# Optimization experiments

Hardware: AMD Instinct MI355X
Metric: run time of the kernel (lower is better)

The kernel has to match this reference:

```python
import jax, jax.numpy as jnp
import numpy as np

B, T, H, NH, K = 8, 1024, 1024, 16, 3
HD = H // NH
EPS = 1e-5


def _ln(x, g, b):
    m = jnp.mean(x, axis=-1, keepdims=True)
    v = jnp.mean((x - m) ** 2, axis=-1, keepdims=True)
    return (x - m) * jax.lax.rsqrt(v + EPS) * g + b


def _ffn(x, g, b, w1, b1, w2, b2):
    h = jax.nn.gelu(_ln(x, g, b) @ w1 + b1, approximate=False)
    return h @ w2 + b2


def setup_inputs() -> dict:
    key = jax.random.key(0)
    ks = jax.random.split(key, 10)
    s = 0.02
    d = {}
    d['x'] = jax.random.normal(ks[0], (B, T, H), jnp.float32)
    d['ln1_g'] = jnp.ones((H,), jnp.float32); d['ln1_b'] = jnp.zeros((H,), jnp.float32)
    d['ffn1_w1'] = jax.random.normal(ks[1], (H, 2 * H), jnp.float32) * s
    d['ffn1_b1'] = jnp.zeros((2 * H,), jnp.float32)
    d['ffn1_w2'] = jax.random.normal(ks[2], (2 * H, H), jnp.float32) * s
    d['ffn1_b2'] = jnp.zeros((H,), jnp.float32)
    d['an_g'] = jnp.ones((H,), jnp.float32); d['an_b'] = jnp.zeros((H,), jnp.float32)
    d['qkv_w'] = jax.random.normal(ks[3], (H, 3 * H), jnp.float32) * s
    d['qkv_b'] = jnp.zeros((3 * H,), jnp.float32)
    d['out_w'] = jax.random.normal(ks[4], (H, H), jnp.float32) * s
    d['out_b'] = jnp.zeros((H,), jnp.float32)
    d['cn_g'] = jnp.ones((H,), jnp.float32); d['cn_b'] = jnp.zeros((H,), jnp.float32)
    d['dw_k'] = jax.random.normal(ks[5], (H, 1, K), jnp.float32) * s  # depthwise [O,I/g,K]
    d['dw_b'] = jnp.zeros((H,), jnp.float32)
    d['pw_w'] = jax.random.normal(ks[6], (H, H), jnp.float32) * s  # pointwise [out,in]
    d['pw_b'] = jnp.zeros((H,), jnp.float32)
    d['ln2_g'] = jnp.ones((H,), jnp.float32); d['ln2_b'] = jnp.zeros((H,), jnp.float32)
    d['ffn2_w1'] = jax.random.normal(ks[7], (H, 2 * H), jnp.float32) * s
    d['ffn2_b1'] = jnp.zeros((2 * H,), jnp.float32)
    d['ffn2_w2'] = jax.random.normal(ks[8], (2 * H, H), jnp.float32) * s
    d['ffn2_b2'] = jnp.zeros((H,), jnp.float32)
    return d


def reference(x, ln1_g, ln1_b, ffn1_w1, ffn1_b1, ffn1_w2, ffn1_b2,
              an_g, an_b, qkv_w, qkv_b, out_w, out_b,
              cn_g, cn_b, dw_k, dw_b, pw_w, pw_b,
              ln2_g, ln2_b, ffn2_w1, ffn2_b1, ffn2_w2, ffn2_b2):
    # macaron FFN 1
    x = x + 0.5 * _ffn(x, ln1_g, ln1_b, ffn1_w1, ffn1_b1, ffn1_w2, ffn1_b2)

    # causal self-attention (pre-norm)
    h = _ln(x, an_g, an_b)
    qkv = (h @ qkv_w + qkv_b).reshape(B, T, 3, NH, HD)
    q, k, v = qkv[:, :, 0], qkv[:, :, 1], qkv[:, :, 2]  # [B,T,NH,HD]
    scale = 1.0 / np.sqrt(HD).astype(np.float32)
    scores = jnp.einsum('bqhd,bkhd->bhqk', q, k) * scale  # [B,NH,T,T]
    causal = jnp.tril(jnp.ones((T, T), dtype=bool))
    scores = jnp.where(causal[None, None], scores, -jnp.inf)
    attn = jax.nn.softmax(scores, axis=-1)
    o = jnp.einsum('bhqk,bkhd->bqhd', attn, v).reshape(B, T, H)
    x = x + (o @ out_w + out_b)

    # conv module: LN -> causal depthwise conv(k=3) -> GELU -> pointwise conv
    c = _ln(x, cn_g, cn_b).transpose(0, 2, 1)  # [B,H,T]
    c = jnp.pad(c, ((0, 0), (0, 0), (K - 1, 0)))  # causal left pad
    c = jax.lax.conv_general_dilated(
        c, dw_k, window_strides=(1,), padding='VALID',
        dimension_numbers=('NCH', 'OIH', 'NCH'), feature_group_count=H)
    c = c + dw_b[None, :, None]
    c = jax.nn.gelu(c, approximate=False)
    c = jnp.einsum('oc,bct->bot', pw_w, c) + pw_b[None, :, None]  # 1x1 conv
    x = x + c.transpose(0, 2, 1)

    # macaron FFN 2
    x = x + 0.5 * _ffn(x, ln2_g, ln2_b, ffn2_w1, ffn2_b1, ffn2_w2, ffn2_b2)
    return x
```

## Files before the change

### kernel.cpp

```cpp
#include <hip/hip_runtime.h>
#include <hip/hip_bf16.h>
#include <math.h>

typedef __bf16 bf16;
typedef __bf16 bf16x8 __attribute__((ext_vector_type(8)));
typedef float  f32x4  __attribute__((ext_vector_type(4)));

#define B_   8
#define T_   1024
#define H_   1024
#define MTOK (B_ * T_)

static __device__ __forceinline__ float gelu_f(float x) {
    return 0.5f * x * (1.0f + erff(x * 0.70710678118654752f));
}

static __device__ __forceinline__ void async16(const bf16* g, bf16* l) {
    __builtin_amdgcn_global_load_lds(
        (const __attribute__((address_space(1))) void*)g,
        (__attribute__((address_space(3))) void*)l, 16, 0, 0);
}

__global__ __launch_bounds__(256)
void transpose_cast_k(const float* __restrict__ in, bf16* __restrict__ out,
                      int Kd, int Nd)
{
    __shared__ float tile[32][33];
    int n0 = blockIdx.x * 32;
    int k0 = blockIdx.y * 32;
    int tx = threadIdx.x & 31, ty = threadIdx.x >> 5;
#pragma unroll
    for (int i = 0; i < 32; i += 8)
        tile[ty + i][tx] = in[(size_t)(k0 + ty + i) * Nd + n0 + tx];
    __syncthreads();
#pragma unroll
    for (int i = 0; i < 32; i += 8)
        out[(size_t)(n0 + ty + i) * Kd + k0 + tx] = (bf16)tile[tx][ty + i];
}

__global__ __launch_bounds__(256)
void cast_k(const float* __restrict__ in, bf16* __restrict__ out)
{
    int i = blockIdx.x * 256 + threadIdx.x;
    float4 v = ((const float4*)in)[i];
    bf16* o = out + (size_t)i * 4;
    o[0] = (bf16)v.x; o[1] = (bf16)v.y; o[2] = (bf16)v.z; o[3] = (bf16)v.w;
}

__global__ __launch_bounds__(256)
void transpose_v_k(const bf16* __restrict__ qkv, bf16* __restrict__ vt)
{
    __shared__ bf16 tile[64][72];
    const int t0 = blockIdx.x * 64;
    const int bh = blockIdx.y;
    const int b = bh >> 4, h = bh & 15;
    const int tid = threadIdx.x;
#pragma unroll
    for (int i = 0; i < 2; i++) {
        int c = tid + i * 256;
        int row = c >> 3, ch = (c & 7) << 3;
        *(bf16x8*)(&tile[row][ch]) =
            *(const bf16x8*)(&qkv[(size_t)(b * T_ + t0 + row) * 3072 + 2048 + h * 64 + ch]);
    }
    __syncthreads();
#pragma unroll
    for (int i = 0; i < 2; i++) {
        int c = tid + i * 256;
        int hd = c >> 3, tc = (c & 7) << 3;
        bf16x8 v;
#pragma unroll
        for (int j = 0; j < 8; j++) v[j] = tile[tc + j][hd];
        *(bf16x8*)(&vt[((size_t)bh * 64 + hd) * T_ + t0 + tc]) = v;
    }
}

__global__ __launch_bounds__(256)
void ln_k(const float* __restrict__ x, const float* __restrict__ g,
          const float* __restrict__ b, bf16* __restrict__ out)
{
    int row = blockIdx.x;
    float4 v = ((const float4*)(x + (size_t)row * H_))[threadIdx.x];
    float s  = v.x + v.y + v.z + v.w;
    float s2 = v.x * v.x + v.y * v.y + v.z * v.z + v.w * v.w;
#pragma unroll
    for (int off = 32; off > 0; off >>= 1) {
        s  += __shfl_down(s, off);
        s2 += __shfl_down(s2, off);
    }
    __shared__ float red[8];
    int wave = threadIdx.x >> 6, lane = threadIdx.x & 63;
    if (lane == 0) { red[wave] = s; red[wave + 4] = s2; }
    __syncthreads();
    s  = red[0] + red[1] + red[2] + red[3];
    s2 = red[4] + red[5] + red[6] + red[7];
    float mean = s * (1.0f / H_);
    float var  = s2 * (1.0f / H_) - mean * mean;
    float rstd = rsqrtf(var + 1e-5f);
    int c = threadIdx.x * 4;
    float4 gv = *(const float4*)(g + c);
    float4 bv = *(const float4*)(b + c);
    bf16* o = out + (size_t)row * H_ + c;
    o[0] = (bf16)((v.x - mean) * rstd * gv.x + bv.x);
    o[1] = (bf16)((v.y - mean) * rstd * gv.y + bv.y);
    o[2] = (bf16)((v.z - mean) * rstd * gv.z + bv.z);
    o[3] = (bf16)((v.w - mean) * rstd * gv.w + bv.w);
}

__global__ __launch_bounds__(256)
void dwconv_k(const bf16* __restrict__ cl, const float* __restrict__ kw,
              const float* __restrict__ kb, bf16* __restrict__ out)
{
    size_t idx = (size_t)blockIdx.x * 256 + threadIdx.x;
    int ch = (int)(idx & (H_ - 1));
    int t  = (int)((idx >> 10) & (T_ - 1));
    float acc = kb[ch];
    float w0 = kw[ch * 3 + 0], w1 = kw[ch * 3 + 1], w2 = kw[ch * 3 + 2];
    acc += (float)cl[idx] * w2;
    if (t >= 1) acc += (float)cl[idx - H_] * w1;
    if (t >= 2) acc += (float)cl[idx - 2 * H_] * w0;
    out[idx] = (bf16)gelu_f(acc);
}

template<int EPI>
__global__ __launch_bounds__(256)
void gemm_k(const bf16* __restrict__ A, const bf16* __restrict__ WT,
            const float* __restrict__ bias, const float* __restrict__ res,
            float* __restrict__ outF, bf16* __restrict__ outB,
            int N, int K)
{
    __shared__ __align__(16) bf16 As[2][128 * 32];
    __shared__ __align__(16) bf16 Bs[2][128 * 32];
    const int tid  = threadIdx.x;
    const int wave = tid >> 6;
    const int lane = tid & 63;
    const int quad = lane >> 4;
    const int lr   = lane & 15;
    const int bm = blockIdx.x * 128;
    const int bn = blockIdx.y * 128;
    const int wm = (wave & 1) * 64;
    const int wn = (wave >> 1) * 64;

    const int crow = lane >> 2;
    const int ccol = (lane & 3) << 3;

    auto stage = [&](int k0, int buf) {
#pragma unroll
        for (int t = 0; t < 2; t++) {
            const int c = wave * 2 + t;
            async16(&A[(size_t)(bm + c * 16 + crow) * K + k0 + ccol], &As[buf][c * 512]);
            async16(&WT[(size_t)(bn + c * 16 + crow) * K + k0 + ccol], &Bs[buf][c * 512]);
        }
    };

    f32x4 acc[4][4];
#pragma unroll
    for (int mi = 0; mi < 4; mi++)
#pragma unroll
        for (int ni = 0; ni < 4; ni++)
#pragma unroll
            for (int r = 0; r < 4; r++) acc[mi][ni][r] = 0.f;

    stage(0, 0);
    __syncthreads();
    const int nk = K >> 5;
    for (int ki = 0; ki < nk; ki++) {
        const int cur = ki & 1;
        if (ki + 1 < nk) stage((ki + 1) << 5, cur ^ 1);

        bf16x8 af[4], bfr[4];
#pragma unroll
        for (int mi = 0; mi < 4; mi++)
            af[mi] = *(const bf16x8*)(&As[cur][(wm + mi * 16 + lr) * 32 + quad * 8]);
#pragma unroll
        for (int ni = 0; ni < 4; ni++)
            bfr[ni] = *(const bf16x8*)(&Bs[cur][(wn + ni * 16 + lr) * 32 + quad * 8]);
#pragma unroll
        for (int mi = 0; mi < 4; mi++)
#pragma unroll
            for (int ni = 0; ni < 4; ni++)
                acc[mi][ni] = __builtin_amdgcn_mfma_f32_16x16x32_bf16(
                    af[mi], bfr[ni], acc[mi][ni], 0, 0, 0);
        __syncthreads();
    }

#pragma unroll
    for (int mi = 0; mi < 4; mi++) {
#pragma unroll
        for (int ni = 0; ni < 4; ni++) {
            int col = bn + wn + ni * 16 + lr;
            float bv = bias[col];
#pragma unroll
            for (int r = 0; r < 4; r++) {
                int row = bm + wm + mi * 16 + quad * 4 + r;
                size_t idx = (size_t)row * N + col;
                float v = acc[mi][ni][r] + bv;
                if (EPI == 0)      outB[idx] = (bf16)gelu_f(v);
                else if (EPI == 1) outB[idx] = (bf16)v;
                else if (EPI == 2) outF[idx] = v + res[idx];
                else               outF[idx] = res[idx] + 0.5f * v;
            }
        }
    }
}

template<int EPI>
__global__ __launch_bounds__(256)
void gemm64_k(const bf16* __restrict__ A, const bf16* __restrict__ WT,
              const float* __restrict__ bias, const float* __restrict__ res,
              float* __restrict__ outF, bf16* __restrict__ outB,
              int N, int K)
{
    __shared__ __align__(16) bf16 As[2][64 * 32];
    __shared__ __align__(16) bf16 Bs[2][128 * 32];
    const int tid  = threadIdx.x;
    const int wave = tid >> 6;
    const int lane = tid & 63;
    const int quad = lane >> 4;
    const int lr   = lane & 15;
    const int bm = blockIdx.x * 64;
    const int bn = blockIdx.y * 128;
    const int wm = (wave & 1) * 32;
    const int wn = (wave >> 1) * 64;

    const int crow = lane >> 2;
    const int ccol = (lane & 3) << 3;

    auto stage = [&](int k0, int buf) {
        async16(&A[(size_t)(bm + wave * 16 + crow) * K + k0 + ccol], &As[buf][wave * 512]);
#pragma unroll
        for (int t = 0; t < 2; t++) {
            const int c = wave * 2 + t;
            async16(&WT[(size_t)(bn + c * 16 + crow) * K + k0 + ccol], &Bs[buf][c * 512]);
        }
    };

    f32x4 acc[2][4];
#pragma unroll
    for (int mi = 0; mi < 2; mi++)
#pragma unroll
        for (int ni = 0; ni < 4; ni++)
#pragma unroll
            for (int r = 0; r < 4; r++) acc[mi][ni][r] = 0.f;

    stage(0, 0);
    __syncthreads();
    const int nk = K >> 5;
    for (int ki = 0; ki < nk; ki++) {
        const int cur = ki & 1;
        if (ki + 1 < nk) stage((ki + 1) << 5, cur ^ 1);

        bf16x8 af[2], bfr[4];
#pragma unroll
        for (int mi = 0; mi < 2; mi++)
            af[mi] = *(const bf16x8*)(&As[cur][(wm + mi * 16 + lr) * 32 + quad * 8]);
#pragma unroll
        for (int ni = 0; ni < 4; ni++)
            bfr[ni] = *(const bf16x8*)(&Bs[cur][(wn + ni * 16 + lr) * 32 + quad * 8]);
#pragma unroll
        for (int mi = 0; mi < 2; mi++)
#pragma unroll
            for (int ni = 0; ni < 4; ni++)
                acc[mi][ni] = __builtin_amdgcn_mfma_f32_16x16x32_bf16(
                    af[mi], bfr[ni], acc[mi][ni], 0, 0, 0);
        __syncthreads();
    }

#pragma unroll
    for (int mi = 0; mi < 2; mi++) {
#pragma unroll
        for (int ni = 0; ni < 4; ni++) {
            int col = bn + wn + ni * 16 + lr;
            float bv = bias[col];
#pragma unroll
            for (int r = 0; r < 4; r++) {
                int row = bm + wm + mi * 16 + quad * 4 + r;
                size_t idx = (size_t)row * N + col;
                float v = acc[mi][ni][r] + bv;
                if (EPI == 0)      outB[idx] = (bf16)gelu_f(v);
                else if (EPI == 1) outB[idx] = (bf16)v;
                else if (EPI == 2) outF[idx] = v + res[idx];
                else               outF[idx] = res[idx] + 0.5f * v;
            }
        }
    }
}

__global__ __launch_bounds__(256)
void attn_k(const bf16* __restrict__ qkv, const bf16* __restrict__ vt,
            bf16* __restrict__ o)
{
    const int B0 = blockIdx.x;
    const int bh = blockIdx.y;
    const int b = bh >> 4, h = bh & 15;
    const int tid  = threadIdx.x;
    const int wave = tid >> 6, lane = tid & 63;
    const int quad = lane >> 4, lr = lane & 15;

    __shared__ __align__(16) bf16 Ks[2][2][64 * 32];
    __shared__ __align__(16) bf16 Vs[2][2][64 * 32];
    __shared__ __align__(16) bf16 Ps[4][16 * 72];

    const int crow = lane >> 2;
    const int ccol = (lane & 3) << 3;

    const int qa = B0 * 128 + wave * 16;
    const int qb = qa + 64;

    bf16x8 qfa[2], qfb[2];
    {
        const size_t ra = ((size_t)(b * T_ + qa + lr)) * 3072 + h * 64;
        const size_t rb = ((size_t)(b * T_ + qb + lr)) * 3072 + h * 64;
        qfa[0] = *(const bf16x8*)(&qkv[ra + quad * 8]);
        qfa[1] = *(const bf16x8*)(&qkv[ra + 32 + quad * 8]);
        qfb[0] = *(const bf16x8*)(&qkv[rb + quad * 8]);
        qfb[1] = *(const bf16x8*)(&qkv[rb + 32 + quad * 8]);
#pragma unroll
        for (int j = 0; j < 8; j++) {
            qfa[0][j] = (bf16)((float)qfa[0][j] * 0.125f);
            qfa[1][j] = (bf16)((float)qfa[1][j] * 0.125f);
            qfb[0][j] = (bf16)((float)qfb[0][j] * 0.125f);
            qfb[1][j] = (bf16)((float)qfb[1][j] * 0.125f);
        }
    }

    f32x4 oa[4], ob[4];
    float la[4], lb[4];
#pragma unroll
    for (int ni = 0; ni < 4; ni++)
#pragma unroll
        for (int r = 0; r < 4; r++) { oa[ni][r] = 0.f; ob[ni][r] = 0.f; }
#pragma unroll
    for (int r = 0; r < 4; r++) { la[r] = 0.f; lb[r] = 0.f; }

    const size_t kbase = (size_t)b * T_ * 3072 + 1024 + h * 64;
    const size_t vbase = (size_t)bh * 64 * T_;

    auto stage = [&](int kt, int buf) {
#pragma unroll
        for (int half = 0; half < 2; half++) {
            async16(&qkv[kbase + (size_t)(kt * 64 + wave * 16 + crow) * 3072 + half * 32 + ccol],
                    &Ks[buf][half][wave * 512]);
            async16(&vt[vbase + (size_t)(wave * 16 + crow) * T_ + kt * 64 + half * 32 + ccol],
                    &Vs[buf][half][wave * 512]);
        }
    };

    const int ktmax = 2 * B0 + 1;
    stage(0, 0);
    __syncthreads();

    for (int kt = 0; kt <= ktmax; kt++) {
        const int cur = kt & 1;
        if (kt < ktmax) stage(kt + 1, cur ^ 1);

        bf16x8 kf[4][2], vf[4][2];
#pragma unroll
        for (int ni = 0; ni < 4; ni++) {
            kf[ni][0] = *(const bf16x8*)(&Ks[cur][0][(ni * 16 + lr) * 32 + quad * 8]);
            kf[ni][1] = *(const bf16x8*)(&Ks[cur][1][(ni * 16 + lr) * 32 + quad * 8]);
            vf[ni][0] = *(const bf16x8*)(&Vs[cur][0][(ni * 16 + lr) * 32 + quad * 8]);
            vf[ni][1] = *(const bf16x8*)(&Vs[cur][1][(ni * 16 + lr) * 32 + quad * 8]);
        }

        auto stripe = [&](const bf16x8 (&qf)[2], f32x4 (&oacc)[4], float (&lsum)[4],
                          int q0, bool diag) {
            f32x4 sv[4];
#pragma unroll
            for (int ni = 0; ni < 4; ni++) {
                f32x4 t;
#pragma unroll
                for (int r = 0; r < 4; r++) t[r] = 0.f;
                t = __builtin_amdgcn_mfma_f32_16x16x32_bf16(qf[0], kf[ni][0], t, 0, 0, 0);
                t = __builtin_amdgcn_mfma_f32_16x16x32_bf16(qf[1], kf[ni][1], t, 0, 0, 0);
                sv[ni] = t;
            }
            if (diag) {
#pragma unroll
                for (int ni = 0; ni < 4; ni++)
#pragma unroll
                    for (int r = 0; r < 4; r++)
                        if (kt * 64 + ni * 16 + lr > q0 + quad * 4 + r)
                            sv[ni][r] = -INFINITY;
            }
#pragma unroll
            for (int ni = 0; ni < 4; ni++)
#pragma unroll
                for (int r = 0; r < 4; r++) {
                    float p = __expf(sv[ni][r]);
                    lsum[r] += p;
                    Ps[wave][(quad * 4 + r) * 72 + ni * 16 + lr] = (bf16)p;
                }
            bf16x8 pf0 = *(const bf16x8*)(&Ps[wave][lr * 72 + quad * 8]);
            bf16x8 pf1 = *(const bf16x8*)(&Ps[wave][lr * 72 + 32 + quad * 8]);
#pragma unroll
            for (int ni = 0; ni < 4; ni++) {
                oacc[ni] = __builtin_amdgcn_mfma_f32_16x16x32_bf16(pf0, vf[ni][0], oacc[ni], 0, 0, 0);
                oacc[ni] = __builtin_amdgcn_mfma_f32_16x16x32_bf16(pf1, vf[ni][1], oacc[ni], 0, 0, 0);
            }
        };

        if (kt <= 2 * B0)
            stripe(qfa, oa, la, qa, kt == 2 * B0);
        stripe(qfb, ob, lb, qb, kt == ktmax);
        __syncthreads();
    }

#pragma unroll
    for (int off = 1; off < 16; off <<= 1)
#pragma unroll
        for (int r = 0; r < 4; r++) {
            la[r] += __shfl_xor(la[r], off);
            lb[r] += __shfl_xor(lb[r], off);
        }

#pragma unroll
    for (int r = 0; r < 4; r++) {
        float inva = 1.0f / la[r], invb = 1.0f / lb[r];
        int ga = qa + quad * 4 + r, gb = qb + quad * 4 + r;
#pragma unroll
        for (int ni = 0; ni < 4; ni++) {
            o[((size_t)(b * T_ + ga)) * H_ + h * 64 + ni * 16 + lr] = (bf16)(oa[ni][r] * inva);
            o[((size_t)(b * T_ + gb)) * H_ + h * 64 + ni * 16 + lr] = (bf16)(ob[ni][r] * invb);
        }
    }
}

extern "C" void kernel_launch(void* const* d_in, const int* in_sizes, int n_in,
                              void* d_out, int out_size, void* d_ws, size_t ws_size,
                              hipStream_t stream)
{
    const float* x_in  = (const float*)d_in[0];
    const float* ln1_g = (const float*)d_in[1];
    const float* ln1_b = (const float*)d_in[2];
    const float* f1w1  = (const float*)d_in[3];
    const float* f1b1  = (const float*)d_in[4];
    const float* f1w2  = (const float*)d_in[5];
    const float* f1b2  = (const float*)d_in[6];
    const float* an_g  = (const float*)d_in[7];
    const float* an_b  = (const float*)d_in[8];
    const float* qkv_w = (const float*)d_in[9];
    const float* qkv_b = (const float*)d_in[10];
    const float* out_w = (const float*)d_in[11];
    const float* out_b = (const float*)d_in[12];
    const float* cn_g  = (const float*)d_in[13];
    const float* cn_b  = (const float*)d_in[14];
    const float* dw_k  = (const float*)d_in[15];
    const float* dw_b  = (const float*)d_in[16];
    const float* pw_w  = (const float*)d_in[17];
    const float* pw_b  = (const float*)d_in[18];
    const float* ln2_g = (const float*)d_in[19];
    const float* ln2_b = (const float*)d_in[20];
    const float* f2w1  = (const float*)d_in[21];
    const float* f2b1  = (const float*)d_in[22];
    const float* f2w2  = (const float*)d_in[23];
    const float* f2b2  = (const float*)d_in[24];
    float* outp = (float*)d_out;

    char* ws = (char*)d_ws;
    size_t off = 0;
    auto alloc = [&](size_t bytes) {
        char* p = ws + off;
        off += (bytes + 255) & ~(size_t)255;
        return p;
    };
    bf16* w1T_1 = (bf16*)alloc(2048ULL * 1024 * 2);
    bf16* w2T_1 = (bf16*)alloc(1024ULL * 2048 * 2);
    bf16* qkvT  = (bf16*)alloc(3072ULL * 1024 * 2);
    bf16* outT  = (bf16*)alloc(1024ULL * 1024 * 2);
    bf16* pwB   = (bf16*)alloc(1024ULL * 1024 * 2);
    bf16* w1T_2 = (bf16*)alloc(2048ULL * 1024 * 2);
    bf16* w2T_2 = (bf16*)alloc(1024ULL * 2048 * 2);
    bf16* bufa  = (bf16*)alloc((size_t)MTOK * 1024 * 2);
    bf16* gbuf  = (bf16*)alloc((size_t)MTOK * 1024 * 2);
    bf16* hid   = (bf16*)alloc((size_t)MTOK * 3072 * 2);
    float* xw   = (float*)alloc((size_t)MTOK * 1024 * 4);
    bf16* vt    = gbuf;

    transpose_cast_k<<<dim3(64, 32), 256, 0, stream>>>(f1w1, w1T_1, 1024, 2048);
    transpose_cast_k<<<dim3(32, 64), 256, 0, stream>>>(f1w2, w2T_1, 2048, 1024);
    transpose_cast_k<<<dim3(96, 32), 256, 0, stream>>>(qkv_w, qkvT, 1024, 3072);
    transpose_cast_k<<<dim3(32, 32), 256, 0, stream>>>(out_w, outT, 1024, 1024);
    transpose_cast_k<<<dim3(64, 32), 256, 0, stream>>>(f2w1, w1T_2, 1024, 2048);
    transpose_cast_k<<<dim3(32, 64), 256, 0, stream>>>(f2w2, w2T_2, 2048, 1024);
    cast_k<<<1024, 256, 0, stream>>>(pw_w, pwB);

    ln_k<<<MTOK, 256, 0, stream>>>(x_in, ln1_g, ln1_b, bufa);
    gemm_k<0><<<dim3(64, 16), 256, 0, stream>>>(bufa, w1T_1, f1b1, nullptr, nullptr, hid, 2048, 1024);
    gemm64_k<3><<<dim3(128, 8), 256, 0, stream>>>(hid, w2T_1, f1b2, x_in, xw, nullptr, 1024, 2048);

    ln_k<<<MTOK, 256, 0, stream>>>(xw, an_g, an_b, bufa);
    gemm_k<1><<<dim3(64, 24), 256, 0, stream>>>(bufa, qkvT, qkv_b, nullptr, nullptr, hid, 3072, 1024);
    transpose_v_k<<<dim3(16, 128), 256, 0, stream>>>(hid, vt);
    attn_k<<<dim3(8, 128), 256, 0, stream>>>(hid, vt, bufa);
    gemm64_k<2><<<dim3(128, 8), 256, 0, stream>>>(bufa, outT, out_b, xw, xw, nullptr, 1024, 1024);

    ln_k<<<MTOK, 256, 0, stream>>>(xw, cn_g, cn_b, bufa);
    dwconv_k<<<MTOK * 1024 / 256, 256, 0, stream>>>(bufa, dw_k, dw_b, gbuf);
    gemm64_k<2><<<dim3(128, 8), 256, 0, stream>>>(gbuf, pwB, pw_b, xw, xw, nullptr, 1024, 1024);

    ln_k<<<MTOK, 256, 0, stream>>>(xw, ln2_g, ln2_b, bufa);
    gemm_k<0><<<dim3(64, 16), 256, 0, stream>>>(bufa, w1T_2, f2b1, nullptr, nullptr, hid, 2048, 1024);
    gemm64_k<3><<<dim3(128, 8), 256, 0, stream>>>(hid, w2T_2, f2b2, xw, outp, nullptr, 1024, 2048);
}
```

Baseline: 683.0 us.

## Fuse weight prep, write V transposed from QKV GEMM, restructure attention loop

Merges the seven weight transpose/cast launches into a single table-driven prep kernel. The QKV GEMM epilogue now writes V directly in transposed layout and pre-scales Q by 1/8, which removes the separate V-transpose kernel and the in-attention Q scaling. The attention kernel launches its heaviest causal blocks first. It also drops double-buffered K/V staging in favour of a single buffer with barriers around each load, which halves shared memory but exposes load latency.

```diff
diff --git a/kernel.cpp b/kernel.cpp
--- a/kernel.cpp
+++ b/kernel.cpp
@@ -3,6 +3,7 @@
 #include <math.h>
 
 typedef __bf16 bf16;
+typedef __bf16 bf16x4 __attribute__((ext_vector_type(4)));
 typedef __bf16 bf16x8 __attribute__((ext_vector_type(8)));
 typedef float  f32x4  __attribute__((ext_vector_type(4)));
 
@@ -21,56 +22,41 @@
         (__attribute__((address_space(3))) void*)l, 16, 0, 0);
 }
 
-__global__ __launch_bounds__(256)
-void transpose_cast_k(const float* __restrict__ in, bf16* __restrict__ out,
-                      int Kd, int Nd)
+struct PrepTab {
+    const float* in[7];
+    bf16*        out[7];
+    int kd[7], nd[7], mode[7];
+    int bx0[8];
+};
+
+__global__ __launch_bounds__(256)
+void prep_k(PrepTab tab)
 {
     __shared__ float tile[32][33];
-    int n0 = blockIdx.x * 32;
-    int k0 = blockIdx.y * 32;
-    int tx = threadIdx.x & 31, ty = threadIdx.x >> 5;
-#pragma unroll
-    for (int i = 0; i < 32; i += 8)
-        tile[ty + i][tx] = in[(size_t)(k0 + ty + i) * Nd + n0 + tx];
-    __syncthreads();
-#pragma unroll
-    for (int i = 0; i < 32; i += 8)
-        out[(size_t)(n0 + ty + i) * Kd + k0 + tx] = (bf16)tile[tx][ty + i];
-}
-
-__global__ __launch_bounds__(256)
-void cast_k(const float* __restrict__ in, bf16* __restrict__ out)
-{
-    int i = blockIdx.x * 256 + threadIdx.x;
-    float4 v = ((const float4*)in)[i];
-    bf16* o = out + (size_t)i * 4;
-    o[0] = (bf16)v.x; o[1] = (bf16)v.y; o[2] = (bf16)v.z; o[3] = (bf16)v.w;
-}
-
-__global__ __launch_bounds__(256)
-void transpose_v_k(const bf16* __restrict__ qkv, bf16* __restrict__ vt)
-{
-    __shared__ bf16 tile[64][72];
-    const int t0 = blockIdx.x * 64;
-    const int bh = blockIdx.y;
-    const int b = bh >> 4, h = bh & 15;
-    const int tid = threadIdx.x;
-#pragma unroll
-    for (int i = 0; i < 2; i++) {
-        int c = tid + i * 256;
-        int row = c >> 3, ch = (c & 7) << 3;
-        *(bf16x8*)(&tile[row][ch]) =
-            *(const bf16x8*)(&qkv[(size_t)(b * T_ + t0 + row) * 3072 + 2048 + h * 64 + ch]);
-    }
-    __syncthreads();
-#pragma unroll
-    for (int i = 0; i < 2; i++) {
-        int c = tid + i * 256;
-        int hd = c >> 3, tc = (c & 7) << 3;
-        bf16x8 v;
-#pragma unroll
-        for (int j = 0; j < 8; j++) v[j] = tile[tc + j][hd];
-        *(bf16x8*)(&vt[((size_t)bh * 64 + hd) * T_ + t0 + tc]) = v;
+    int bx = blockIdx.x;
+    int j = 0;
+    while (bx >= tab.bx0[j + 1]) j++;
+    int local = bx - tab.bx0[j];
+    const float* in = tab.in[j];
+    bf16* out = tab.out[j];
+    if (tab.mode[j] == 0) {
+        int Kd = tab.kd[j], Nd = tab.nd[j];
+        int nbn = Nd >> 5;
+        int n0 = (local % nbn) * 32;
+        int k0 = (local / nbn) * 32;
+        int tx = threadIdx.x & 31, ty = threadIdx.x >> 5;
+#pragma unroll
+        for (int i = 0; i < 32; i += 8)
+            tile[ty + i][tx] = in[(size_t)(k0 + ty + i) * Nd + n0 + tx];
+        __syncthreads();
+#pragma unroll
+        for (int i = 0; i < 32; i += 8)
+            out[(size_t)(n0 + ty + i) * Kd + k0 + tx] = (bf16)tile[tx][ty + i];
+    } else {
+        size_t i = (size_t)local * 1024 + threadIdx.x * 4;
+        float4 v = *(const float4*)(in + i);
+        bf16* o = out + i;
+        o[0] = (bf16)v.x; o[1] = (bf16)v.y; o[2] = (bf16)v.z; o[3] = (bf16)v.w;
     }
 }
 
@@ -126,7 +112,7 @@
 void gemm_k(const bf16* __restrict__ A, const bf16* __restrict__ WT,
             const float* __restrict__ bias, const float* __restrict__ res,
             float* __restrict__ outF, bf16* __restrict__ outB,
-            int N, int K)
+            bf16* __restrict__ vtp, int N, int K)
 {
     __shared__ __align__(16) bf16 As[2][128 * 32];
     __shared__ __align__(16) bf16 Bs[2][128 * 32];
@@ -189,15 +175,27 @@
         for (int ni = 0; ni < 4; ni++) {
             int col = bn + wn + ni * 16 + lr;
             float bv = bias[col];
-#pragma unroll
-            for (int r = 0; r < 4; r++) {
-                int row = bm + wm + mi * 16 + quad * 4 + r;
-                size_t idx = (size_t)row * N + col;
-                float v = acc[mi][ni][r] + bv;
-                if (EPI == 0)      outB[idx] = (bf16)gelu_f(v);
-                else if (EPI == 1) outB[idx] = (bf16)v;
-                else if (EPI == 2) outF[idx] = v + res[idx];
-                else               outF[idx] = res[idx] + 0.5f * v;
+            if (EPI == 4 && col >= 2048) {
+                int vcol = col - 2048;
+                int hh = vcol >> 6, hd = vcol & 63;
+                int rowbase = bm + wm + mi * 16 + quad * 4;
+                int bq = rowbase >> 10, t0 = rowbase & 1023;
+                bf16x4 tmp;
+#pragma unroll
+                for (int r = 0; r < 4; r++) tmp[r] = (bf16)(acc[mi][ni][r] + bv);
+                *(bf16x4*)(&vtp[((size_t)((bq * 16 + hh) * 64 + hd)) * T_ + t0]) = tmp;
+            } else {
+#pragma unroll
+                for (int r = 0; r < 4; r++) {
+                    int row = bm + wm + mi * 16 + quad * 4 + r;
+                    size_t idx = (size_t)row * N + col;
+                    float v = acc[mi][ni][r] + bv;
+                    if (EPI == 0)      outB[idx] = (bf16)gelu_f(v);
+                    else if (EPI == 1) outB[idx] = (bf16)v;
+                    else if (EPI == 2) outF[idx] = v + res[idx];
+                    else if (EPI == 3) outF[idx] = res[idx] + 0.5f * v;
+                    else               outB[idx] = (bf16)(col < 1024 ? v * 0.125f : v);
+                }
             }
         }
     }
@@ -289,15 +287,15 @@
 void attn_k(const bf16* __restrict__ qkv, const bf16* __restrict__ vt,
             bf16* __restrict__ o)
 {
-    const int B0 = blockIdx.x;
+    const int B0 = 7 - blockIdx.x;
     const int bh = blockIdx.y;
     const int b = bh >> 4, h = bh & 15;
     const int tid  = threadIdx.x;
     const int wave = tid >> 6, lane = tid & 63;
     const int quad = lane >> 4, lr = lane & 15;
 
-    __shared__ __align__(16) bf16 Ks[2][2][64 * 32];
-    __shared__ __align__(16) bf16 Vs[2][2][64 * 32];
+    __shared__ __align__(16) bf16 Ks[2][64 * 32];
+    __shared__ __align__(16) bf16 Vs[2][64 * 32];
     __shared__ __align__(16) bf16 Ps[4][16 * 72];
 
     const int crow = lane >> 2;
@@ -314,13 +312,6 @@
         qfa[1] = *(const bf16x8*)(&qkv[ra + 32 + quad * 8]);
         qfb[0] = *(const bf16x8*)(&qkv[rb + quad * 8]);
         qfb[1] = *(const bf16x8*)(&qkv[rb + 32 + quad * 8]);
-#pragma unroll
-        for (int j = 0; j < 8; j++) {
-            qfa[0][j] = (bf16)((float)qfa[0][j] * 0.125f);
-            qfa[1][j] = (bf16)((float)qfa[1][j] * 0.125f);
-            qfb[0][j] = (bf16)((float)qfb[0][j] * 0.125f);
-            qfb[1][j] = (bf16)((float)qfb[1][j] * 0.125f);
-        }
     }
 
     f32x4 oa[4], ob[4];
@@ -335,74 +326,65 @@
     const size_t kbase = (size_t)b * T_ * 3072 + 1024 + h * 64;
     const size_t vbase = (size_t)bh * 64 * T_;
 
-    auto stage = [&](int kt, int buf) {
+    auto stripe = [&](const bf16x8 (&qf)[2], f32x4 (&oacc)[4], float (&lsum)[4],
+                      int q0, int kcol0, bool diag) {
+        bf16x8 kf0[4], kf1[4];
+#pragma unroll
+        for (int ni = 0; ni < 4; ni++) {
+            kf0[ni] = *(const bf16x8*)(&Ks[0][(ni * 16 + lr) * 32 + quad * 8]);
+            kf1[ni] = *(const bf16x8*)(&Ks[1][(ni * 16 + lr) * 32 + quad * 8]);
+        }
+        f32x4 sv[4];
+#pragma unroll
+        for (int ni = 0; ni < 4; ni++) {
+            f32x4 t;
+#pragma unroll
+            for (int r = 0; r < 4; r++) t[r] = 0.f;
+            t = __builtin_amdgcn_mfma_f32_16x16x32_bf16(qf[0], kf0[ni], t, 0, 0, 0);
+            t = __builtin_amdgcn_mfma_f32_16x16x32_bf16(qf[1], kf1[ni], t, 0, 0, 0);
+            sv[ni] = t;
+        }
+        if (diag) {
+#pragma unroll
+            for (int ni = 0; ni < 4; ni++)
+#pragma unroll
+                for (int r = 0; r < 4; r++)
+                    if (kcol0 + ni * 16 + lr > q0 + quad * 4 + r)
+                        sv[ni][r] = -INFINITY;
+        }
+#pragma unroll
+        for (int ni = 0; ni < 4; ni++)
+#pragma unroll
+            for (int r = 0; r < 4; r++) {
+                float p = __expf(sv[ni][r]);
+                lsum[r] += p;
+                Ps[wave][(quad * 4 + r) * 72 + ni * 16 + lr] = (bf16)p;
+            }
+        bf16x8 pf0 = *(const bf16x8*)(&Ps[wave][lr * 72 + quad * 8]);
+        bf16x8 pf1 = *(const bf16x8*)(&Ps[wave][lr * 72 + 32 + quad * 8]);
+#pragma unroll
+        for (int ni = 0; ni < 4; ni++) {
+            bf16x8 vf0 = *(const bf16x8*)(&Vs[0][(ni * 16 + lr) * 32 + quad * 8]);
+            bf16x8 vf1 = *(const bf16x8*)(&Vs[1][(ni * 16 + lr) * 32 + quad * 8]);
+            oacc[ni] = __builtin_amdgcn_mfma_f32_16x16x32_bf16(pf0, vf0, oacc[ni], 0, 0, 0);
+            oacc[ni] = __builtin_amdgcn_mfma_f32_16x16x32_bf16(pf1, vf1, oacc[ni], 0, 0, 0);
+        }
+    };
+
+    const int ktmax = 2 * B0 + 1;
+    for (int kt = 0; kt <= ktmax; kt++) {
+        __syncthreads();
 #pragma unroll
         for (int half = 0; half < 2; half++) {
             async16(&qkv[kbase + (size_t)(kt * 64 + wave * 16 + crow) * 3072 + half * 32 + ccol],
-                    &Ks[buf][half][wave * 512]);
+                    &Ks[half][wave * 512]);
             async16(&vt[vbase + (size_t)(wave * 16 + crow) * T_ + kt * 64 + half * 32 + ccol],
-                    &Vs[buf][half][wave * 512]);
-        }
-    };
-
-    const int ktmax = 2 * B0 + 1;
-    stage(0, 0);
-    __syncthreads();
-
-    for (int kt = 0; kt <= ktmax; kt++) {
-        const int cur = kt & 1;
-        if (kt < ktmax) stage(kt + 1, cur ^ 1);
-
-        bf16x8 kf[4][2], vf[4][2];
-#pragma unroll
-        for (int ni = 0; ni < 4; ni++) {
-            kf[ni][0] = *(const bf16x8*)(&Ks[cur][0][(ni * 16 + lr) * 32 + quad * 8]);
-            kf[ni][1] = *(const bf16x8*)(&Ks[cur][1][(ni * 16 + lr) * 32 + quad * 8]);
-            vf[ni][0] = *(const bf16x8*)(&Vs[cur][0][(ni * 16 + lr) * 32 + quad * 8]);
-            vf[ni][1] = *(const bf16x8*)(&Vs[cur][1][(ni * 16 + lr) * 32 + quad * 8]);
-        }
-
-        auto stripe = [&](const bf16x8 (&qf)[2], f32x4 (&oacc)[4], float (&lsum)[4],
-                          int q0, bool diag) {
-            f32x4 sv[4];
-#pragma unroll
-            for (int ni = 0; ni < 4; ni++) {
-                f32x4 t;
-#pragma unroll
-                for (int r = 0; r < 4; r++) t[r] = 0.f;
-                t = __builtin_amdgcn_mfma_f32_16x16x32_bf16(qf[0], kf[ni][0], t, 0, 0, 0);
-                t = __builtin_amdgcn_mfma_f32_16x16x32_bf16(qf[1], kf[ni][1], t, 0, 0, 0);
-                sv[ni] = t;
-            }
-            if (diag) {
-#pragma unroll
-                for (int ni = 0; ni < 4; ni++)
-#pragma unroll
-                    for (int r = 0; r < 4; r++)
-                        if (kt * 64 + ni * 16 + lr > q0 + quad * 4 + r)
-                            sv[ni][r] = -INFINITY;
-            }
-#pragma unroll
-            for (int ni = 0; ni < 4; ni++)
-#pragma unroll
-                for (int r = 0; r < 4; r++) {
-                    float p = __expf(sv[ni][r]);
-                    lsum[r] += p;
-                    Ps[wave][(quad * 4 + r) * 72 + ni * 16 + lr] = (bf16)p;
-                }
-            bf16x8 pf0 = *(const bf16x8*)(&Ps[wave][lr * 72 + quad * 8]);
-            bf16x8 pf1 = *(const bf16x8*)(&Ps[wave][lr * 72 + 32 + quad * 8]);
-#pragma unroll
-            for (int ni = 0; ni < 4; ni++) {
-                oacc[ni] = __builtin_amdgcn_mfma_f32_16x16x32_bf16(pf0, vf[ni][0], oacc[ni], 0, 0, 0);
-                oacc[ni] = __builtin_amdgcn_mfma_f32_16x16x32_bf16(pf1, vf[ni][1], oacc[ni], 0, 0, 0);
-            }
-        };
-
+                    &Vs[half][wave * 512]);
+        }
+        __syncthreads();
         if (kt <= 2 * B0)
-            stripe(qfa, oa, la, qa, kt == 2 * B0);
-        stripe(qfb, ob, lb, qb, kt == ktmax);
-        __syncthreads();
+            stripe(qfa, oa, la, qa, kt * 64, kt == 2 * B0);
+        stripe(qfb, ob, lb, qb, kt * 64, kt == ktmax);
     }
 
 #pragma unroll
@@ -476,21 +458,28 @@
     float* xw   = (float*)alloc((size_t)MTOK * 1024 * 4);
     bf16* vt    = gbuf;
 
-    transpose_cast_k<<<dim3(64, 32), 256, 0, stream>>>(f1w1, w1T_1, 1024, 2048);
-    transpose_cast_k<<<dim3(32, 64), 256, 0, stream>>>(f1w2, w2T_1, 2048, 1024);
-    transpose_cast_k<<<dim3(96, 32), 256, 0, stream>>>(qkv_w, qkvT, 1024, 3072);
-    transpose_cast_k<<<dim3(32, 32), 256, 0, stream>>>(out_w, outT, 1024, 1024);
-    transpose_cast_k<<<dim3(64, 32), 256, 0, stream>>>(f2w1, w1T_2, 1024, 2048);
-    transpose_cast_k<<<dim3(32, 64), 256, 0, stream>>>(f2w2, w2T_2, 2048, 1024);
-    cast_k<<<1024, 256, 0, stream>>>(pw_w, pwB);
+    PrepTab tab;
+    tab.in[0] = f1w1;  tab.out[0] = w1T_1; tab.kd[0] = 1024; tab.nd[0] = 2048; tab.mode[0] = 0;
+    tab.in[1] = f1w2;  tab.out[1] = w2T_1; tab.kd[1] = 2048; tab.nd[1] = 1024; tab.mode[1] = 0;
+    tab.in[2] = qkv_w; tab.out[2] = qkvT;  tab.kd[2] = 1024; tab.nd[2] = 3072; tab.mode[2] = 0;
+    tab.in[3] = out_w; tab.out[3] = outT;  tab.kd[3] = 1024; tab.nd[3] = 1024; tab.mode[3] = 0;
+    tab.in[4] = f2w1;  tab.out[4] = w1T_2; tab.kd[4] = 1024; tab.nd[4] = 2048; tab.mode[4] = 0;
+    tab.in[5] = f2w2;  tab.out[5] = w2T_2; tab.kd[5] = 2048; tab.nd[5] = 1024; tab.mode[5] = 0;
+    tab.in[6] = pw_w;  tab.out[6] = pwB;   tab.kd[6] = 1024; tab.nd[6] = 1024; tab.mode[6] = 1;
+    tab.bx0[0] = 0;
+    for (int j = 0; j < 7; j++) {
+        int blocks = tab.mode[j] ? (tab.kd[j] * tab.nd[j] / 1024)
+                                 : (tab.kd[j] / 32) * (tab.nd[j] / 32);
+        tab.bx0[j + 1] = tab.bx0[j] + blocks;
+    }
+    prep_k<<<tab.bx0[7], 256, 0, stream>>>(tab);
 
     ln_k<<<MTOK, 256, 0, stream>>>(x_in, ln1_g, ln1_b, bufa);
-    gemm_k<0><<<dim3(64, 16), 256, 0, stream>>>(bufa, w1T_1, f1b1, nullptr, nullptr, hid, 2048, 1024);
+    gemm_k<0><<<dim3(64, 16), 256, 0, stream>>>(bufa, w1T_1, f1b1, nullptr, nullptr, hid, nullptr, 2048, 1024);
     gemm64_k<3><<<dim3(128, 8), 256, 0, stream>>>(hid, w2T_1, f1b2, x_in, xw, nullptr, 1024, 2048);
 
     ln_k<<<MTOK, 256, 0, stream>>>(xw, an_g, an_b, bufa);
-    gemm_k<1><<<dim3(64, 24), 256, 0, stream>>>(bufa, qkvT, qkv_b, nullptr, nullptr, hid, 3072, 1024);
-    transpose_v_k<<<dim3(16, 128), 256, 0, stream>>>(hid, vt);
+    gemm_k<4><<<dim3(64, 24), 256, 0, stream>>>(bufa, qkvT, qkv_b, nullptr, nullptr, hid, vt, 3072, 1024);
     attn_k<<<dim3(8, 128), 256, 0, stream>>>(hid, vt, bufa);
     gemm64_k<2><<<dim3(128, 8), 256, 0, stream>>>(bufa, outT, out_b, xw, xw, nullptr, 1024, 1024);
 
@@ -499,6 +488,6 @@
     gemm64_k<2><<<dim3(128, 8), 256, 0, stream>>>(gbuf, pwB, pw_b, xw, xw, nullptr, 1024, 1024);
 
     ln_k<<<MTOK, 256, 0, stream>>>(xw, ln2_g, ln2_b, bufa);
-    gemm_k<0><<<dim3(64, 16), 256, 0, stream>>>(bufa, w1T_2, f2b1, nullptr, nullptr, hid, 2048, 1024);
+    gemm_k<0><<<dim3(64, 16), 256, 0, stream>>>(bufa, w1T_2, f2b1, nullptr, nullptr, hid, nullptr, 2048, 1024);
     gemm64_k<3><<<dim3(128, 8), 256, 0, stream>>>(hid, w2T_2, f2b2, xw, outp, nullptr, 1024, 2048);
 }
```

Measured after the change: 666.6 us. 1.02x faster.
